# Kernel tuning notes

Measured on AMD Instinct MI355X. Metric: run time of the kernel, lower is better.

## Reference

```python
import jax, jax.numpy as jnp
import numpy as np

N = 50000
E = 800000
IN_DIM = 128
HID = 32
HEADS = 2
OUT_DIM = 32
EPS = 1e-5          # BatchNorm eps
SLOPE = 0.2         # LeakyReLU negative slope (PyG GATConv default)


def gat_conv(x, src, dst, W, a_src, a_dst, bias, heads, out_dim, concat):
    """PyG-style GATConv (self-loops already appended to src/dst)."""
    n = x.shape[0]
    h = (x @ W).reshape(n, heads, out_dim)            # [N, H, D]
    # per-node attention contributions  [N, H]
    e_src = jnp.sum(h * a_src, axis=-1)
    e_dst = jnp.sum(h * a_dst, axis=-1)
    # per-edge logits [Etot, H]
    e = jax.nn.leaky_relu(e_src[src] + e_dst[dst], SLOPE)
    # segment softmax over destination node
    emax = jax.ops.segment_max(e, dst, num_segments=n)
    emax = jnp.where(jnp.isfinite(emax), emax, 0.0)
    ex = jnp.exp(e - emax[dst])
    denom = jax.ops.segment_sum(ex, dst, num_segments=n)
    alpha = ex / (denom[dst] + 1e-16)                 # [Etot, H]
    # weighted message aggregation
    out = jax.ops.segment_sum(alpha[:, :, None] * h[src], dst, num_segments=n)
    out = out.reshape(n, heads * out_dim) if concat else out.mean(axis=1)
    return out + bias


def batch_norm(x, gamma, beta):
    # training-mode BatchNorm1d over the node (batch) dimension, biased var
    mu = x.mean(axis=0)
    var = x.var(axis=0)
    return (x - mu) * jax.lax.rsqrt(var + EPS) * gamma + beta


def setup_inputs() -> dict:
    key = jax.random.key(0)
    ks = jax.random.split(key, 12)
    s = 0.1
    return {
        "x": jax.random.normal(ks[0], (N, IN_DIM), jnp.float32),
        "W1": jax.random.normal(ks[1], (IN_DIM, HEADS * HID), jnp.float32) * s,
        "as1": jax.random.normal(ks[2], (HEADS, HID), jnp.float32) * s,
        "ad1": jax.random.normal(ks[3], (HEADS, HID), jnp.float32) * s,
        "b1": jnp.zeros((HEADS * HID,), jnp.float32),
        "g1": jnp.ones((HEADS * HID,), jnp.float32),
        "be1": jnp.zeros((HEADS * HID,), jnp.float32),
        "W2": jax.random.normal(ks[4], (HEADS * HID, HEADS * HID), jnp.float32) * s,
        "as2": jax.random.normal(ks[5], (HEADS, HID), jnp.float32) * s,
        "ad2": jax.random.normal(ks[6], (HEADS, HID), jnp.float32) * s,
        "b2": jnp.zeros((HEADS * HID,), jnp.float32),
        "g2": jnp.ones((HEADS * HID,), jnp.float32),
        "be2": jnp.zeros((HEADS * HID,), jnp.float32),
        "W3": jax.random.normal(ks[7], (HEADS * HID, OUT_DIM), jnp.float32) * s,
        "as3": jax.random.normal(ks[8], (1, OUT_DIM), jnp.float32) * s,
        "ad3": jax.random.normal(ks[9], (1, OUT_DIM), jnp.float32) * s,
        "b3": jnp.zeros((OUT_DIM,), jnp.float32),
        "g3": jnp.ones((OUT_DIM,), jnp.float32),
        "be3": jnp.zeros((OUT_DIM,), jnp.float32),
        "edge_index": jax.random.randint(ks[10], (2, E), 0, N, jnp.int64 if jax.config.jax_enable_x64 else jnp.int32),
    }


def reference(x, W1, as1, ad1, b1, g1, be1,
              W2, as2, ad2, b2, g2, be2,
              W3, as3, ad3, b3, g3, be3, edge_index):
    n = x.shape[0]
    loops = jnp.arange(n, dtype=edge_index.dtype)
    src = jnp.concatenate([edge_index[0], loops])  # add_self_loops=True
    dst = jnp.concatenate([edge_index[1], loops])
    h = gat_conv(x, src, dst, W1, as1, ad1, b1, HEADS, HID, True)
    h = jax.nn.relu(batch_norm(h, g1, be1))
    h = gat_conv(h, src, dst, W2, as2, ad2, b2, HEADS, HID, True)
    h = jax.nn.relu(batch_norm(h, g2, be2))
    h = gat_conv(h, src, dst, W3, as3, ad3, b3, 1, OUT_DIM, False)
    h = jax.nn.relu(batch_norm(h, g3, be3))
    return h
```

## Files before the change

kernel.cpp:

```cpp
#include <hip/hip_runtime.h>


__device__ __forceinline__ float lrelu(float x) { return x > 0.f ? x : 0.2f * x; }
__device__ __forceinline__ unsigned short f2bf(float x) {
    unsigned u = __float_as_uint(x);
    return (unsigned short)((u + 0x7FFFu + ((u >> 16) & 1u)) >> 16);
}
__device__ __forceinline__ float bf2f(unsigned short v) {
    return __uint_as_float(((unsigned)v) << 16);
}

template <int K, int OUTF, int H, bool FUSE>
__global__ __launch_bounds__(256) void gemm_attn_k(
    const float* __restrict__ in, const float* __restrict__ W,
    const float* __restrict__ scale, const float* __restrict__ shift,
    const float* __restrict__ a_src, const float* __restrict__ a_dst,
    unsigned short* __restrict__ hb, float* __restrict__ es,
    float* __restrict__ ed, int N)
{
    constexpr int BK = 32;
    constexpr int M = 128;
    constexpr int XS = BK + 4;
    constexpr int HS = OUTF / 32;
    __shared__ float xs[M * XS];
    __shared__ float wsl[32 * XS];
    __shared__ float redS[8 * 132];
    __shared__ float redD[8 * 132];

    const int tid = threadIdx.x;
    const int tile = (HS == 2) ? (blockIdx.x >> 1) : blockIdx.x;
    const int hs = (HS == 2) ? (blockIdx.x & 1) : 0;
    const int n0 = tile * M;
    const int jb = hs * 32;

    float acc[4][4];
#pragma unroll
    for (int i = 0; i < 4; ++i)
#pragma unroll
        for (int jj = 0; jj < 4; ++jj) acc[i][jj] = 0.f;

    const int lane = tid & 31;
    const int jt = (tid >> 5) * 4;

    for (int kc = 0; kc < K; kc += BK) {
#pragma unroll
        for (int i = 0; i < 4; ++i) {
            int f = i * 256 + tid;
            int n = f >> 3;
            int kq = f & 7;
            int gn = n0 + n;
            if (gn >= N) gn = N - 1;
            float4 v = *(const float4*)(in + (size_t)gn * K + kc + kq * 4);
            if constexpr (FUSE) {
                float4 sc = *(const float4*)(scale + kc + kq * 4);
                float4 sh = *(const float4*)(shift + kc + kq * 4);
                v.x = fmaxf(v.x * sc.x + sh.x, 0.f);
                v.y = fmaxf(v.y * sc.y + sh.y, 0.f);
                v.z = fmaxf(v.z * sc.z + sh.z, 0.f);
                v.w = fmaxf(v.w * sc.w + sh.w, 0.f);
            }
            *(float4*)&xs[n * XS + kq * 4] = v;
        }
        {
            int g = tid;
#pragma unroll
            for (int i = 0; i < 4; ++i, g += 256) {
                int j = g & 31;
                int kl = g >> 5;
                wsl[j * XS + kl] = W[(size_t)(kc + kl) * OUTF + jb + j];
            }
        }
        __syncthreads();
#pragma unroll
        for (int k4 = 0; k4 < BK; k4 += 4) {
            float4 xv[4];
#pragma unroll
            for (int i = 0; i < 4; ++i)
                xv[i] = *(float4*)&xs[(lane + 32 * i) * XS + k4];
#pragma unroll
            for (int jj = 0; jj < 4; ++jj) {
                float4 wv = *(float4*)&wsl[(jt + jj) * XS + k4];
#pragma unroll
                for (int i = 0; i < 4; ++i)
                    acc[i][jj] += xv[i].x * wv.x + xv[i].y * wv.y
                                + xv[i].z * wv.z + xv[i].w * wv.w;
            }
        }
        __syncthreads();
    }

    const int jg = tid >> 5;
#pragma unroll
    for (int i = 0; i < 4; ++i) {
        int r = lane + 32 * i;
        int gn = n0 + r;
        float p = 0.f, q = 0.f;
#pragma unroll
        for (int jj = 0; jj < 4; ++jj) {
            p += acc[i][jj] * a_src[jb + jt + jj];
            q += acc[i][jj] * a_dst[jb + jt + jj];
        }
        if (gn < N) {
            uint2 u;
            u.x = (unsigned)f2bf(acc[i][0]) | ((unsigned)f2bf(acc[i][1]) << 16);
            u.y = (unsigned)f2bf(acc[i][2]) | ((unsigned)f2bf(acc[i][3]) << 16);
            *(uint2*)(hb + (size_t)gn * OUTF + jb + jt) = u;
        }
        redS[jg * 132 + r] = p;
        redD[jg * 132 + r] = q;
    }
    __syncthreads();
    if (tid < M) {
        int gn = n0 + tid;
        if (gn < N) {
            float e = 0.f, d = 0.f;
#pragma unroll
            for (int g = 0; g < 8; ++g) {
                e += redS[g * 132 + tid];
                d += redD[g * 132 + tid];
            }
            es[gn * H + hs] = e;
            ed[gn * H + hs] = d;
        }
    }
}

__global__ __launch_bounds__(256) void deg_k(
    const int* __restrict__ ei, int* __restrict__ deg, int E, int N)
{
    int e = blockIdx.x * 256 + threadIdx.x;
    int Et = E + N;
    if (e >= Et) return;
    int d = (e < E) ? ei[E + e] : e - E;
    atomicAdd(&deg[d], 1);
}

__global__ __launch_bounds__(256) void scan1_k(
    const int* __restrict__ deg, int* __restrict__ rowtmp,
    int* __restrict__ bsum, int N)
{
    __shared__ int ls[256];
    int i = blockIdx.x * 256 + threadIdx.x;
    int v = (i < N) ? deg[i] : 0;
    int x = v;
    ls[threadIdx.x] = x;
    __syncthreads();
#pragma unroll
    for (int ofs = 1; ofs < 256; ofs <<= 1) {
        int y = (threadIdx.x >= ofs) ? ls[threadIdx.x - ofs] : 0;
        __syncthreads();
        x += y;
        ls[threadIdx.x] = x;
        __syncthreads();
    }
    if (i < N) rowtmp[i] = x - v;
    if (threadIdx.x == 255) bsum[blockIdx.x] = x;
}

__global__ __launch_bounds__(256) void scan2_k(
    const int* __restrict__ bsum, int* __restrict__ boff, int nb)
{
    __shared__ int ls[256];
    int i = threadIdx.x;
    int v = (i < nb) ? bsum[i] : 0;
    int x = v;
    ls[i] = x;
    __syncthreads();
#pragma unroll
    for (int ofs = 1; ofs < 256; ofs <<= 1) {
        int y = (i >= ofs) ? ls[i - ofs] : 0;
        __syncthreads();
        x += y;
        ls[i] = x;
        __syncthreads();
    }
    if (i < nb) boff[i] = x - v;
}

__global__ __launch_bounds__(256) void scan3_k(
    const int* __restrict__ rowtmp, const int* __restrict__ boff,
    int* __restrict__ rowptr, int N, int Et)
{
    int i = blockIdx.x * 256 + threadIdx.x;
    if (i < N) rowptr[i] = rowtmp[i] + boff[blockIdx.x];
    if (i == 0) rowptr[N] = Et;
}

__global__ __launch_bounds__(256) void scatter_k(
    const int* __restrict__ ei, const int* __restrict__ rowptr,
    int* __restrict__ cur, int* __restrict__ col, int E, int N)
{
    int e = blockIdx.x * 256 + threadIdx.x;
    int Et = E + N;
    if (e >= Et) return;
    int s, d;
    if (e < E) { s = ei[e]; d = ei[E + e]; } else { s = e - E; d = s; }
    int pos = atomicAdd(&cur[d], 1);
    col[rowptr[d] + pos] = s;
}

template <int H>
__global__ __launch_bounds__(256) void node_sg_k(
    const int* __restrict__ rowptr, const int* __restrict__ col,
    const float* __restrict__ es, const float* __restrict__ ed,
    const unsigned short* __restrict__ hb, float* __restrict__ out,
    float* __restrict__ psum, float* __restrict__ psumsq, int N)
{
    constexpr int LPN = H * 16;
    constexpr int F = LPN * 2;
    constexpr int NPB = 256 / LPN;
    int t = blockIdx.x * 256 + threadIdx.x;
    int node = t / LPN;
    int lane = t - node * LPN;
    const bool valid = node < N;

    const uint* h2 = (const uint*)hb;
    const float2* es2 = (const float2*)es;

    int base = 0, deg = 0;
    float ed0 = 0.f, ed1 = 0.f;
    if (valid) {
        base = rowptr[node];
        deg = rowptr[node + 1] - base;
        if constexpr (H == 2) {
            float2 e = ((const float2*)ed)[node];
            ed0 = e.x; ed1 = e.y;
        } else {
            ed0 = ed[node];
        }
    }

    int sc_ = 0;
    float x0 = 0.f, x1 = 0.f;
    if (lane < deg) {
        sc_ = col[base + lane];
        if constexpr (H == 2) {
            float2 v = es2[sc_];
            x0 = __expf(lrelu(v.x + ed0));
            x1 = __expf(lrelu(v.y + ed1));
        } else {
            x0 = __expf(lrelu(es[sc_] + ed0));
        }
    }
    float s0 = x0, s1 = x1;
    for (int e = lane + LPN; e < deg; e += LPN) {
        int s = col[base + e];
        if constexpr (H == 2) {
            float2 v = es2[s];
            s0 += __expf(lrelu(v.x + ed0));
            s1 += __expf(lrelu(v.y + ed1));
        } else {
            s0 += __expf(lrelu(es[s] + ed0));
        }
    }
#pragma unroll
    for (int m = LPN / 2; m; m >>= 1) {
        s0 += __shfl_xor(s0, m, LPN);
        if (H == 2) s1 += __shfl_xor(s1, m, LPN);
    }
    float rd0 = 1.f / (s0 + 1e-16f);
    float rd1 = (H == 2) ? 1.f / (s1 + 1e-16f) : 0.f;

    const bool hi = (H == 2) && (lane >= 16);
    float acc0 = 0.f, acc1 = 0.f;
    int dcap = deg < LPN ? deg : LPN;
    int e = 0;
    for (; e + 8 <= dcap; e += 8) {
        int sI[8];
        float a[8];
#pragma unroll
        for (int u = 0; u < 8; ++u) {
            sI[u] = __shfl(sc_, e + u, LPN);
            float a0 = __shfl(x0, e + u, LPN);
            if constexpr (H == 2) {
                float a1 = __shfl(x1, e + u, LPN);
                a[u] = hi ? a1 * rd1 : a0 * rd0;
            } else {
                a[u] = a0 * rd0;
            }
        }
        uint v[8];
#pragma unroll
        for (int u = 0; u < 8; ++u) v[u] = h2[(size_t)sI[u] * LPN + lane];
#pragma unroll
        for (int u = 0; u < 8; ++u) {
            acc0 += a[u] * bf2f((unsigned short)v[u]);
            acc1 += a[u] * bf2f((unsigned short)(v[u] >> 16));
        }
    }
    for (; e + 4 <= dcap; e += 4) {
        int sI[4];
        float a[4];
#pragma unroll
        for (int u = 0; u < 4; ++u) {
            sI[u] = __shfl(sc_, e + u, LPN);
            float a0 = __shfl(x0, e + u, LPN);
            if constexpr (H == 2) {
                float a1 = __shfl(x1, e + u, LPN);
                a[u] = hi ? a1 * rd1 : a0 * rd0;
            } else {
                a[u] = a0 * rd0;
            }
        }
        uint v[4];
#pragma unroll
        for (int u = 0; u < 4; ++u) v[u] = h2[(size_t)sI[u] * LPN + lane];
#pragma unroll
        for (int u = 0; u < 4; ++u) {
            acc0 += a[u] * bf2f((unsigned short)v[u]);
            acc1 += a[u] * bf2f((unsigned short)(v[u] >> 16));
        }
    }
    for (; e < dcap; ++e) {
        int sI = __shfl(sc_, e, LPN);
        float a0 = __shfl(x0, e, LPN);
        float a;
        if constexpr (H == 2) {
            float a1 = __shfl(x1, e, LPN);
            a = hi ? a1 * rd1 : a0 * rd0;
        } else {
            a = a0 * rd0;
        }
        uint v = h2[(size_t)sI * LPN + lane];
        acc0 += a * bf2f((unsigned short)v);
        acc1 += a * bf2f((unsigned short)(v >> 16));
    }
    for (int e2 = LPN; e2 < deg; ++e2) {
        int s = col[base + e2];
        float a;
        if constexpr (H == 2) {
            float2 vv = es2[s];
            a = hi ? __expf(lrelu(vv.y + ed1)) * rd1
                   : __expf(lrelu(vv.x + ed0)) * rd0;
        } else {
            a = __expf(lrelu(es[s] + ed0)) * rd0;
        }
        uint v = h2[(size_t)s * LPN + lane];
        acc0 += a * bf2f((unsigned short)v);
        acc1 += a * bf2f((unsigned short)(v >> 16));
    }
    if (valid)
        ((float2*)out)[(size_t)node * LPN + lane] = make_float2(acc0, acc1);

    __shared__ float ls0[256], ls1[256];
    ls0[threadIdx.x] = acc0;
    ls1[threadIdx.x] = acc1;
    __syncthreads();
    if (threadIdx.x < LPN) {
        int l = threadIdx.x;
        float t0 = 0.f, t0q = 0.f, t1 = 0.f, t1q = 0.f;
#pragma unroll
        for (int g = 0; g < NPB; ++g) {
            float v0 = ls0[g * LPN + l], v1 = ls1[g * LPN + l];
            t0 += v0; t0q += v0 * v0;
            t1 += v1; t1q += v1 * v1;
        }
        int slot = (blockIdx.x & 127) * F;
        atomicAdd(&psum[slot + 2 * l], t0);
        atomicAdd(&psum[slot + 2 * l + 1], t1);
        atomicAdd(&psumsq[slot + 2 * l], t0q);
        atomicAdd(&psumsq[slot + 2 * l + 1], t1q);
    }
}

__global__ void bn_final_k(float* __restrict__ psum,
                           float* __restrict__ psumsq,
                           const float* __restrict__ gamma,
                           const float* __restrict__ beta,
                           float* __restrict__ scale, float* __restrict__ shift,
                           int N, int F)
{
    int f = threadIdx.x;
    if (f >= F) return;
    float s = 0.f, s2 = 0.f;
    for (int b = 0; b < 128; ++b) {
        s += psum[b * F + f];
        s2 += psumsq[b * F + f];
        psum[b * F + f] = 0.f;
        psumsq[b * F + f] = 0.f;
    }
    float inv = 1.f / (float)N;
    float mu = s * inv;
    float var = s2 * inv - mu * mu;
    var = fmaxf(var, 0.f);
    float rs = rsqrtf(var + 1e-5f);
    float sc = rs * gamma[f];
    scale[f] = sc;
    shift[f] = beta[f] - mu * sc;
}

__global__ __launch_bounds__(256) void out_final_k(
    const float* __restrict__ x, const float* __restrict__ scale,
    const float* __restrict__ shift, float* __restrict__ out, int total)
{
    int i = blockIdx.x * 256 + threadIdx.x;
    if (i >= total) return;
    int f = i & 31;
    out[i] = fmaxf(x[i] * scale[f] + shift[f], 0.f);
}


extern "C" void kernel_launch(void* const* d_in, const int* in_sizes, int n_in,
                              void* d_out, int out_size, void* d_ws,
                              size_t ws_size, hipStream_t stream)
{
    const float* x   = (const float*)d_in[0];
    const float* W1  = (const float*)d_in[1];
    const float* as1 = (const float*)d_in[2];
    const float* ad1 = (const float*)d_in[3];
    const float* g1  = (const float*)d_in[5];
    const float* be1 = (const float*)d_in[6];
    const float* W2  = (const float*)d_in[7];
    const float* as2 = (const float*)d_in[8];
    const float* ad2 = (const float*)d_in[9];
    const float* g2  = (const float*)d_in[11];
    const float* be2 = (const float*)d_in[12];
    const float* W3  = (const float*)d_in[13];
    const float* as3 = (const float*)d_in[14];
    const float* ad3 = (const float*)d_in[15];
    const float* g3  = (const float*)d_in[17];
    const float* be3 = (const float*)d_in[18];
    const int*   ei  = (const int*)d_in[19];

    const int N  = in_sizes[0] / 128;
    const int E  = in_sizes[19] / 2;
    const int Et = E + N;
    const int nb = (N + 255) / 256;

    float* ws = (float*)d_ws;
    size_t off = 0;
    unsigned short* Hb = (unsigned short*)(ws + off); off += (size_t)N * 32;
    float* AGG = ws + off;  off += (size_t)N * 64;
    float* ES  = ws + off;  off += (size_t)N * 2;
    float* ED  = ws + off;  off += (size_t)N * 2;
    float* SC  = ws + off;  off += 64;
    float* SH  = ws + off;  off += 64;
    float* PS  = ws + off;  off += (size_t)128 * 64;
    float* PS2 = ws + off;  off += (size_t)128 * 64;
    int* deg    = (int*)(ws + off);  off += N;
    int* cur    = (int*)(ws + off);  off += N;
    int* rowtmp = (int*)(ws + off);  off += N;
    int* bsum   = (int*)(ws + off);  off += 256;
    int* boff   = (int*)(ws + off);  off += 256;
    int* rowptr = (int*)(ws + off);  off += (size_t)N + 1;
    int* col    = (int*)(ws + off);  off += (size_t)Et;

    const int tiles      = (N + 127) / 128;
    const int gemm2Blocks = tiles * 2;
    const int gemm1Blocks = tiles;
    const int sg64Blocks = (int)(((size_t)N * 32 + 255) / 256);
    const int sg32Blocks = (int)(((size_t)N * 16 + 255) / 256);
    const int edgeBlocks = (Et + 255) / 256;
    const int n32Blocks  = (N * 32 + 255) / 256;

    hipMemsetAsync(deg, 0, (size_t)(2 * N) * sizeof(int), stream);
    hipMemsetAsync(PS, 0, (size_t)2 * 128 * 64 * sizeof(float), stream);
    deg_k<<<edgeBlocks, 256, 0, stream>>>(ei, deg, E, N);
    scan1_k<<<nb, 256, 0, stream>>>(deg, rowtmp, bsum, N);
    scan2_k<<<1, 256, 0, stream>>>(bsum, boff, nb);
    scan3_k<<<nb, 256, 0, stream>>>(rowtmp, boff, rowptr, N, Et);
    scatter_k<<<edgeBlocks, 256, 0, stream>>>(ei, rowptr, cur, col, E, N);

    gemm_attn_k<128, 64, 2, false><<<gemm2Blocks, 256, 0, stream>>>(
        x, W1, nullptr, nullptr, as1, ad1, Hb, ES, ED, N);
    node_sg_k<2><<<sg64Blocks, 256, 0, stream>>>(rowptr, col, ES, ED, Hb, AGG, PS, PS2, N);
    bn_final_k<<<1, 64, 0, stream>>>(PS, PS2, g1, be1, SC, SH, N, 64);

    gemm_attn_k<64, 64, 2, true><<<gemm2Blocks, 256, 0, stream>>>(
        AGG, W2, SC, SH, as2, ad2, Hb, ES, ED, N);
    node_sg_k<2><<<sg64Blocks, 256, 0, stream>>>(rowptr, col, ES, ED, Hb, AGG, PS, PS2, N);
    bn_final_k<<<1, 64, 0, stream>>>(PS, PS2, g2, be2, SC, SH, N, 64);

    gemm_attn_k<64, 32, 1, true><<<gemm1Blocks, 256, 0, stream>>>(
        AGG, W3, SC, SH, as3, ad3, Hb, ES, ED, N);
    node_sg_k<1><<<sg32Blocks, 256, 0, stream>>>(rowptr, col, ES, ED, Hb, AGG, PS, PS2, N);
    bn_final_k<<<1, 32, 0, stream>>>(PS, PS2, g3, be3, SC, SH, N, 32);
    out_final_k<<<n32Blocks, 256, 0, stream>>>(AGG, SC, SH, (float*)d_out, N * 32);
}
```

Baseline: 346.7 us.

## Fuse CSR scatter with first GEMM launch and parallelize BN finalize

The edge scatter that builds the CSR column array and the first-layer GEMM+attention kernel become one launch, with block index selecting which role a block plays. Since they are independent, this removes a launch and lets the memory-bound scatter atomics overlap with the GEMM compute. Separately, bn_final now uses 256 threads, each reducing a strided subset of the 128 partial slots, then combines the subsets through shared memory, which shortens the serial 128-step loop. The fused kernel carries the GEMM's shared-memory footprint even for scatter blocks, which may lower occupancy for those blocks.

```diff
diff --git a/kernel.cpp b/kernel.cpp
--- a/kernel.cpp
+++ b/kernel.cpp
@@ -11,8 +11,8 @@
 }
 
 template <int K, int OUTF, int H, bool FUSE>
-__global__ __launch_bounds__(256) void gemm_attn_k(
-    const float* __restrict__ in, const float* __restrict__ W,
+__device__ __forceinline__ void gemm_attn_body(
+    int vbid, const float* __restrict__ in, const float* __restrict__ W,
     const float* __restrict__ scale, const float* __restrict__ shift,
     const float* __restrict__ a_src, const float* __restrict__ a_dst,
     unsigned short* __restrict__ hb, float* __restrict__ es,
@@ -28,8 +28,8 @@
     __shared__ float redD[8 * 132];
 
     const int tid = threadIdx.x;
-    const int tile = (HS == 2) ? (blockIdx.x >> 1) : blockIdx.x;
-    const int hs = (HS == 2) ? (blockIdx.x & 1) : 0;
+    const int tile = (HS == 2) ? (vbid >> 1) : vbid;
+    const int hs = (HS == 2) ? (vbid & 1) : 0;
     const int n0 = tile * M;
     const int jb = hs * 32;
 
@@ -125,6 +125,41 @@
     }
 }
 
+template <int K, int OUTF, int H, bool FUSE>
+__global__ __launch_bounds__(256) void gemm_attn_k(
+    const float* __restrict__ in, const float* __restrict__ W,
+    const float* __restrict__ scale, const float* __restrict__ shift,
+    const float* __restrict__ a_src, const float* __restrict__ a_dst,
+    unsigned short* __restrict__ hb, float* __restrict__ es,
+    float* __restrict__ ed, int N)
+{
+    gemm_attn_body<K, OUTF, H, FUSE>(blockIdx.x, in, W, scale, shift,
+                                     a_src, a_dst, hb, es, ed, N);
+}
+
+template <int K, int OUTF, int H>
+__global__ __launch_bounds__(256) void scatter_gemm_k(
+    const int* __restrict__ ei, const int* __restrict__ rowptr,
+    int* __restrict__ cur, int* __restrict__ col, int E, int SB,
+    const float* __restrict__ in, const float* __restrict__ W,
+    const float* __restrict__ a_src, const float* __restrict__ a_dst,
+    unsigned short* __restrict__ hb, float* __restrict__ es,
+    float* __restrict__ ed, int N)
+{
+    if (blockIdx.x < SB) {
+        int e = blockIdx.x * 256 + threadIdx.x;
+        int Et = E + N;
+        if (e >= Et) return;
+        int s, d;
+        if (e < E) { s = ei[e]; d = ei[E + e]; } else { s = e - E; d = s; }
+        int pos = atomicAdd(&cur[d], 1);
+        col[rowptr[d] + pos] = s;
+        return;
+    }
+    gemm_attn_body<K, OUTF, H, false>(blockIdx.x - SB, in, W, nullptr, nullptr,
+                                      a_src, a_dst, hb, es, ed, N);
+}
+
 __global__ __launch_bounds__(256) void deg_k(
     const int* __restrict__ ei, int* __restrict__ deg, int E, int N)
 {
@@ -184,19 +219,6 @@
     int i = blockIdx.x * 256 + threadIdx.x;
     if (i < N) rowptr[i] = rowtmp[i] + boff[blockIdx.x];
     if (i == 0) rowptr[N] = Et;
-}
-
-__global__ __launch_bounds__(256) void scatter_k(
-    const int* __restrict__ ei, const int* __restrict__ rowptr,
-    int* __restrict__ cur, int* __restrict__ col, int E, int N)
-{
-    int e = blockIdx.x * 256 + threadIdx.x;
-    int Et = E + N;
-    if (e >= Et) return;
-    int s, d;
-    if (e < E) { s = ei[e]; d = ei[E + e]; } else { s = e - E; d = s; }
-    int pos = atomicAdd(&cur[d], 1);
-    col[rowptr[d] + pos] = s;
 }
 
 template <int H>
@@ -370,23 +392,31 @@
                            float* __restrict__ scale, float* __restrict__ shift,
                            int N, int F)
 {
-    int f = threadIdx.x;
-    if (f >= F) return;
+    int f = threadIdx.x % F;
+    int r = threadIdx.x / F;
+    int R = 256 / F;
     float s = 0.f, s2 = 0.f;
-    for (int b = 0; b < 128; ++b) {
+    for (int b = r; b < 128; b += R) {
         s += psum[b * F + f];
         s2 += psumsq[b * F + f];
         psum[b * F + f] = 0.f;
         psumsq[b * F + f] = 0.f;
     }
-    float inv = 1.f / (float)N;
-    float mu = s * inv;
-    float var = s2 * inv - mu * mu;
-    var = fmaxf(var, 0.f);
-    float rs = rsqrtf(var + 1e-5f);
-    float sc = rs * gamma[f];
-    scale[f] = sc;
-    shift[f] = beta[f] - mu * sc;
+    __shared__ float l1[256], l2[256];
+    l1[threadIdx.x] = s;
+    l2[threadIdx.x] = s2;
+    __syncthreads();
+    if (r == 0) {
+        for (int g = 1; g < R; ++g) { s += l1[g * F + f]; s2 += l2[g * F + f]; }
+        float inv = 1.f / (float)N;
+        float mu = s * inv;
+        float var = s2 * inv - mu * mu;
+        var = fmaxf(var, 0.f);
+        float rs = rsqrtf(var + 1e-5f);
+        float sc = rs * gamma[f];
+        scale[f] = sc;
+        shift[f] = beta[f] - mu * sc;
+    }
 }
 
 __global__ __launch_bounds__(256) void out_final_k(
@@ -459,21 +489,22 @@
     scan1_k<<<nb, 256, 0, stream>>>(deg, rowtmp, bsum, N);
     scan2_k<<<1, 256, 0, stream>>>(bsum, boff, nb);
     scan3_k<<<nb, 256, 0, stream>>>(rowtmp, boff, rowptr, N, Et);
-    scatter_k<<<edgeBlocks, 256, 0, stream>>>(ei, rowptr, cur, col, E, N);
-
-    gemm_attn_k<128, 64, 2, false><<<gemm2Blocks, 256, 0, stream>>>(
-        x, W1, nullptr, nullptr, as1, ad1, Hb, ES, ED, N);
+
+    scatter_gemm_k<128, 64, 2><<<edgeBlocks + gemm2Blocks, 256, 0, stream>>>(
+        ei, rowptr, cur, col, E, edgeBlocks,
+        x, W1, as1, ad1, Hb, ES, ED, N);
+
     node_sg_k<2><<<sg64Blocks, 256, 0, stream>>>(rowptr, col, ES, ED, Hb, AGG, PS, PS2, N);
-    bn_final_k<<<1, 64, 0, stream>>>(PS, PS2, g1, be1, SC, SH, N, 64);
+    bn_final_k<<<1, 256, 0, stream>>>(PS, PS2, g1, be1, SC, SH, N, 64);
 
     gemm_attn_k<64, 64, 2, true><<<gemm2Blocks, 256, 0, stream>>>(
         AGG, W2, SC, SH, as2, ad2, Hb, ES, ED, N);
     node_sg_k<2><<<sg64Blocks, 256, 0, stream>>>(rowptr, col, ES, ED, Hb, AGG, PS, PS2, N);
-    bn_final_k<<<1, 64, 0, stream>>>(PS, PS2, g2, be2, SC, SH, N, 64);
+    bn_final_k<<<1, 256, 0, stream>>>(PS, PS2, g2, be2, SC, SH, N, 64);
 
     gemm_attn_k<64, 32, 1, true><<<gemm1Blocks, 256, 0, stream>>>(
         AGG, W3, SC, SH, as3, ad3, Hb, ES, ED, N);
     node_sg_k<1><<<sg32Blocks, 256, 0, stream>>>(rowptr, col, ES, ED, Hb, AGG, PS, PS2, N);
-    bn_final_k<<<1, 32, 0, stream>>>(PS, PS2, g3, be3, SC, SH, N, 32);
+    bn_final_k<<<1, 256, 0, stream>>>(PS, PS2, g3, be3, SC, SH, N, 32);
     out_final_k<<<n32Blocks, 256, 0, stream>>>(AGG, SC, SH, (float*)d_out, N * 32);
 }
```

Measured after the change: 344.9 us. Within noise of the previous version (-0.5%).
